# Performance work log

Hardware: AMD Instinct MI355X
Metric: run time of the kernel (lower is better)

Reference implementation:

```python
import jax, jax.numpy as jnp
import numpy as np

N = 8192
NUM_FEAT = 512
NUM_HIDDENS = 128


def _mlp_params(key, fin, fh):
    k1, k2, k3, k4 = jax.random.split(key, 4)
    s1 = 1.0 / np.sqrt(fin)
    s2 = 1.0 / np.sqrt(fh)
    W1 = jax.random.uniform(k1, (fin, fh), jnp.float32, -s1, s1)
    b1 = jax.random.uniform(k2, (fh,), jnp.float32, -s1, s1)
    W2 = jax.random.uniform(k3, (fh, fh), jnp.float32, -s2, s2)
    b2 = jax.random.uniform(k4, (fh,), jnp.float32, -s2, s2)
    return W1, b1, W2, b2


def setup_inputs() -> dict:
    key = jax.random.key(0)
    ks = jax.random.split(key, 9)
    feat = jax.random.normal(ks[0], (N, NUM_FEAT), jnp.float32)
    adj = jax.random.uniform(ks[1], (N, N), jnp.float32)
    aa = jax.random.uniform(ks[2], (N, N), jnp.float32)
    mod = jax.random.normal(ks[3], (N, N), jnp.float32)
    Wl1, bl1, Wl2, bl2 = _mlp_params(ks[4], NUM_FEAT, NUM_HIDDENS)
    Wu1, bu1, Wu2, bu2 = _mlp_params(ks[5], NUM_FEAT, NUM_HIDDENS)
    Wa1, ba1, Wa2, ba2 = _mlp_params(ks[6], NUM_FEAT, NUM_HIDDENS)
    Wm1, bm1, Wm2, bm2 = _mlp_params(ks[7], NUM_FEAT, NUM_HIDDENS)
    ws = jnp.zeros((3,), jnp.float32)  # nn.init.zeros_(weighted_sum)
    return dict(feat=feat, adj=adj, aa=aa, mod=mod,
                Wl1=Wl1, bl1=bl1, Wl2=Wl2, bl2=bl2,
                Wu1=Wu1, bu1=bu1, Wu2=Wu2, bu2=bu2,
                Wa1=Wa1, ba1=ba1, Wa2=Wa2, ba2=ba2,
                Wm1=Wm1, bm1=bm1, Wm2=Wm2, bm2=bm2,
                ws=ws)


def _latent(feat, W1, b1, W2, b2):
    h = jax.nn.relu(feat @ W1 + b1)
    return h @ W2 + b2  # [N, H]


def reference(feat, adj, aa, mod,
              Wl1, bl1, Wl2, bl2,
              Wu1, bu1, Wu2, bu2,
              Wa1, ba1, Wa2, ba2,
              Wm1, bm1, Wm2, bm2, ws):
    lat_link = _latent(feat, Wl1, bl1, Wl2, bl2)
    lat_aa = _latent(feat, Wa1, ba1, Wa2, ba2)
    lat_mod = _latent(feat, Wm1, bm1, Wm2, bm2)
    lat_unlink = _latent(feat, Wu1, bu1, Wu2, bu2)

    link_ctx = jax.nn.sigmoid(lat_link @ lat_link.T)          # [N, N]
    aa_ctx = jax.nn.sigmoid((lat_aa @ lat_aa.T) * aa)         # [N, N]
    mod_ctx = jax.nn.sigmoid((lat_mod @ lat_mod.T) * mod)     # [N, N]

    w = jax.nn.softmax(ws)  # [3]
    # cat(..., dim=2) @ w  ==  weighted sum of the three contexts
    weight_link = w[0] * link_ctx + w[1] * aa_ctx + w[2] * mod_ctx

    weight_unlink = jax.nn.sigmoid(lat_unlink @ lat_unlink.T)
    return (weight_link - weight_unlink) * adj + weight_unlink
```

## Files before the change

kernel.cpp:

```cpp
#include <hip/hip_runtime.h>


typedef __attribute__((ext_vector_type(8))) short short8;
typedef __attribute__((ext_vector_type(4))) float f32x4;

__device__ __forceinline__ unsigned short f2bf(float x) {
  union { float f; unsigned u; } v; v.f = x;
  unsigned u = v.u + 0x7FFFu + ((v.u >> 16) & 1u);
  return (unsigned short)(u >> 16);
}

__device__ __forceinline__ float sigf(float x) {
  float e = __builtin_amdgcn_exp2f(-1.4426950408889634f * x);
  return __builtin_amdgcn_rcpf(1.0f + e);
}

__device__ __forceinline__ void gload_lds16(const float* g, float* l) {
  __builtin_amdgcn_global_load_lds(
      (const __attribute__((address_space(1))) void*)g,
      (__attribute__((address_space(3))) void*)l, 16, 0, 0);
}
__device__ __forceinline__ void gload_lds16u(const unsigned short* g, unsigned short* l) {
  __builtin_amdgcn_global_load_lds(
      (const __attribute__((address_space(1))) void*)g,
      (__attribute__((address_space(3))) void*)l, 16, 0, 0);
}

__device__ __forceinline__ unsigned lds_off(const void* p) {
  return (unsigned)(uintptr_t)(const __attribute__((address_space(3))) void*)p;
}
__device__ __forceinline__ f32x4 ds_read_f32x4(unsigned a) {
  f32x4 d;
  asm volatile("ds_read_b128 %0, %1" : "=v"(d) : "v"(a));
  return d;
}
__device__ __forceinline__ short8 ds_read_frag(unsigned a) {
  short8 d;
  asm volatile("ds_read_b128 %0, %1" : "=v"(d) : "v"(a));
  return d;
}

__global__ __launch_bounds__(256) void k_featfrag(const float* __restrict__ feat,
                                                  unsigned short* __restrict__ dst) {
  int t = blockIdx.x * 256 + threadIdx.x;
  int row = t >> 6, kc = t & 63;
  const float4* s = reinterpret_cast<const float4*>(feat + row * 512 + kc * 8);
  float4 v0 = s[0], v1 = s[1];
  short8 o;
  o[0] = f2bf(v0.x); o[1] = f2bf(v0.y); o[2] = f2bf(v0.z); o[3] = f2bf(v0.w);
  o[4] = f2bf(v1.x); o[5] = f2bf(v1.y); o[6] = f2bf(v1.z); o[7] = f2bf(v1.w);
  int mb = row >> 4, kk = kc >> 2;
  int lane = ((kc & 3) << 4) | (row & 15);
  *reinterpret_cast<short8*>(dst + ((size_t)((mb * 16 + kk) * 64 + lane)) * 8) = o;
}

__global__ __launch_bounds__(256) void k_wfrag(
    const float* __restrict__ w1_0, const float* __restrict__ w1_1,
    const float* __restrict__ w1_2, const float* __restrict__ w1_3,
    const float* __restrict__ w2_0, const float* __restrict__ w2_1,
    const float* __restrict__ w2_2, const float* __restrict__ w2_3,
    unsigned short* __restrict__ w1f, unsigned short* __restrict__ w2f) {
  int t = blockIdx.x * 256 + threadIdx.x;
  if (t < 32768) {
    int lane = t & 63, nb = (t >> 6) & 7, kk = (t >> 9) & 15, g = t >> 13;
    const float* W = g == 0 ? w1_0 : g == 1 ? w1_1 : g == 2 ? w1_2 : w1_3;
    int q = lane >> 4, r = lane & 15;
    int col = nb * 16 + r;
    short8 o;
#pragma unroll
    for (int j = 0; j < 8; ++j) o[j] = f2bf(W[(kk * 32 + q * 8 + j) * 128 + col]);
    *reinterpret_cast<short8*>(w1f + (size_t)t * 8) = o;
  } else if (t < 40960) {
    int t2 = t - 32768;
    int lane = t2 & 63, nb = (t2 >> 6) & 7, kk = (t2 >> 9) & 3, g = t2 >> 11;
    const float* W = g == 0 ? w2_0 : g == 1 ? w2_1 : g == 2 ? w2_2 : w2_3;
    int q = lane >> 4, r = lane & 15;
    int col = nb * 16 + r;
    short8 o;
#pragma unroll
    for (int j = 0; j < 8; ++j) o[j] = f2bf(W[(kk * 32 + q * 8 + j) * 128 + col]);
    *reinterpret_cast<short8*>(w2f + (size_t)t2 * 8) = o;
  }
}

__global__ __launch_bounds__(256) void k_gemm1(
    const unsigned short* __restrict__ featf, const unsigned short* __restrict__ w1f,
    const float* __restrict__ b1_0, const float* __restrict__ b1_1,
    const float* __restrict__ b1_2, const float* __restrict__ b1_3,
    unsigned short* __restrict__ hfrag) {
  int bi = blockIdx.x, g = blockIdx.y;
  int lane = threadIdx.x & 63, w = threadIdx.x >> 6;
  int wm = w >> 1, wn = w & 1;
  int q = lane >> 4, r = lane & 15;
  int mbase = 8 * bi + 4 * wm;

  f32x4 s[4][4];
#pragma unroll
  for (int mi = 0; mi < 4; ++mi)
#pragma unroll
    for (int nj = 0; nj < 4; ++nj) s[mi][nj] = (f32x4){0.f, 0.f, 0.f, 0.f};

  for (int kk = 0; kk < 16; ++kk) {
    short8 a[4], b[4];
#pragma unroll
    for (int mi = 0; mi < 4; ++mi)
      a[mi] = *reinterpret_cast<const short8*>(
          featf + ((size_t)(((mbase + mi) * 16 + kk) * 64 + lane)) * 8);
#pragma unroll
    for (int nj = 0; nj < 4; ++nj)
      b[nj] = *reinterpret_cast<const short8*>(
          w1f + ((size_t)(((g * 16 + kk) * 8 + 4 * wn + nj) * 64 + lane)) * 8);
#pragma unroll
    for (int mi = 0; mi < 4; ++mi)
#pragma unroll
      for (int nj = 0; nj < 4; ++nj)
        s[mi][nj] = __builtin_amdgcn_mfma_f32_16x16x32_bf16(a[mi], b[nj], s[mi][nj], 0, 0, 0);
  }

  const float* b1 = g == 0 ? b1_0 : g == 1 ? b1_1 : g == 2 ? b1_2 : b1_3;
#pragma unroll
  for (int nj = 0; nj < 4; ++nj) {
    int cl = 64 * wn + 16 * nj + r;
    float bias = b1[cl];
    int Cg = 128 * g + cl;
    int kkd = Cg >> 5;
    int lane2hi = ((Cg >> 3) & 3) << 4;
    int j2 = Cg & 7;
#pragma unroll
    for (int mi = 0; mi < 4; ++mi) {
#pragma unroll
      for (int v = 0; v < 4; ++v) {
        int R = 128 * bi + 64 * wm + 16 * mi + 4 * q + v;
        float val = fmaxf(s[mi][nj][v] + bias, 0.0f);
        int mb = R >> 4;
        int lane2 = lane2hi | (R & 15);
        hfrag[((size_t)((mb * 16 + kkd) * 64 + lane2)) * 8 + j2] = f2bf(val);
      }
    }
  }
}

__global__ __launch_bounds__(256) void k_gemm2(
    const unsigned short* __restrict__ hfrag, const unsigned short* __restrict__ w2f,
    const float* __restrict__ b2_0, const float* __restrict__ b2_1,
    const float* __restrict__ b2_2, const float* __restrict__ b2_3,
    unsigned short* __restrict__ latf) {
  int bi = blockIdx.x, g = blockIdx.y;
  int lane = threadIdx.x & 63, w = threadIdx.x >> 6;
  int wm = w >> 1, wn = w & 1;
  int q = lane >> 4, r = lane & 15;
  int mbase = 8 * bi + 4 * wm;

  f32x4 s[4][4];
#pragma unroll
  for (int mi = 0; mi < 4; ++mi)
#pragma unroll
    for (int nj = 0; nj < 4; ++nj) s[mi][nj] = (f32x4){0.f, 0.f, 0.f, 0.f};

#pragma unroll
  for (int kk = 0; kk < 4; ++kk) {
    short8 a[4], b[4];
#pragma unroll
    for (int mi = 0; mi < 4; ++mi)
      a[mi] = *reinterpret_cast<const short8*>(
          hfrag + ((size_t)(((mbase + mi) * 16 + 4 * g + kk) * 64 + lane)) * 8);
#pragma unroll
    for (int nj = 0; nj < 4; ++nj)
      b[nj] = *reinterpret_cast<const short8*>(
          w2f + ((size_t)(((g * 4 + kk) * 8 + 4 * wn + nj) * 64 + lane)) * 8);
#pragma unroll
    for (int mi = 0; mi < 4; ++mi)
#pragma unroll
      for (int nj = 0; nj < 4; ++nj)
        s[mi][nj] = __builtin_amdgcn_mfma_f32_16x16x32_bf16(a[mi], b[nj], s[mi][nj], 0, 0, 0);
  }

  const float* b2 = g == 0 ? b2_0 : g == 1 ? b2_1 : g == 2 ? b2_2 : b2_3;
#pragma unroll
  for (int nj = 0; nj < 4; ++nj) {
    int cl = 64 * wn + 16 * nj + r;
    float bias = b2[cl];
    int kkd = cl >> 5;
    int lane2hi = ((cl >> 3) & 3) << 4;
    int j2 = cl & 7;
#pragma unroll
    for (int mi = 0; mi < 4; ++mi) {
#pragma unroll
      for (int v = 0; v < 4; ++v) {
        int R = 128 * bi + 64 * wm + 16 * mi + 4 * q + v;
        float val = s[mi][nj][v] + bias;
        int mb = R >> 4;
        int lane2 = lane2hi | (R & 15);
        latf[((size_t)(((g * 512 + mb) * 4 + kkd) * 64 + lane2)) * 8 + j2] = f2bf(val);
      }
    }
  }
}


#define FJLD(dst, p, OFF) \
  asm volatile("global_load_dwordx4 %0, %1, off offset:" OFF : "=v"(dst) : "v"(p))

#define LOADFJ(F, TJ)                                                         \
  do {                                                                        \
    const unsigned short* _b = latf + (size_t)(TJ) * 2048 + (size_t)lane * 8; \
    FJLD(F[0][0], _b, "0");    FJLD(F[0][1], _b, "1024");                     \
    FJLD(F[0][2], _b, "2048"); FJLD(F[0][3], _b, "3072");                     \
    _b += GS;                                                                 \
    FJLD(F[1][0], _b, "0");    FJLD(F[1][1], _b, "1024");                     \
    FJLD(F[1][2], _b, "2048"); FJLD(F[1][3], _b, "3072");                     \
    _b += GS;                                                                 \
    FJLD(F[2][0], _b, "0");    FJLD(F[2][1], _b, "1024");                     \
    FJLD(F[2][2], _b, "2048"); FJLD(F[2][3], _b, "3072");                     \
    _b += GS;                                                                 \
    FJLD(F[3][0], _b, "0");    FJLD(F[3][1], _b, "1024");                     \
    FJLD(F[3][2], _b, "2048"); FJLD(F[3][3], _b, "3072");                     \
  } while (0)

#define GRAM(FC, G, OUTV)                                                     \
  do {                                                                        \
    short8 _f0 = ds_read_frag(fib + (G * 4 + 0) * 1024u + l16);               \
    short8 _f1 = ds_read_frag(fib + (G * 4 + 1) * 1024u + l16);               \
    short8 _f2 = ds_read_frag(fib + (G * 4 + 2) * 1024u + l16);               \
    short8 _f3 = ds_read_frag(fib + (G * 4 + 3) * 1024u + l16);               \
    asm volatile("s_waitcnt lgkmcnt(0)" ::: "memory");                        \
    __builtin_amdgcn_sched_barrier(0);                                        \
    f32x4 _sg = (f32x4){0.f, 0.f, 0.f, 0.f};                                  \
    _sg = __builtin_amdgcn_mfma_f32_16x16x32_bf16(FC[G][0], _f0, _sg, 0, 0, 0); \
    _sg = __builtin_amdgcn_mfma_f32_16x16x32_bf16(FC[G][1], _f1, _sg, 0, 0, 0); \
    _sg = __builtin_amdgcn_mfma_f32_16x16x32_bf16(FC[G][2], _f2, _sg, 0, 0, 0); \
    _sg = __builtin_amdgcn_mfma_f32_16x16x32_bf16(FC[G][3], _f3, _sg, 0, 0, 0); \
    OUTV = _sg;                                                               \
  } while (0)

#define STEP(S, FC, FN)                                                       \
  do {                                                                        \
    int _sn = ((S) + 1 < 32) ? (S) + 1 : 31;                                  \
    LOADFJ(FN, cs * 128 + _sn * 4 + w);                                       \
    __builtin_amdgcn_sched_barrier(0);                                        \
    {                                                                         \
      int _sf = ((S) + 2 < 32) ? (S) + 2 : 31;                                \
      fill_ew(_sf, ((S) + 2) % 3);                                            \
    }                                                                         \
    __builtin_amdgcn_sched_barrier(0);                                        \
    asm volatile("s_waitcnt vmcnt(23)" ::: "memory");                         \
    __builtin_amdgcn_sched_barrier(0);                                        \
    unsigned _ea = ewb + (unsigned)(((S) % 3) * 3072 + rdidx) * 4u;           \
    f32x4 ewa = ds_read_f32x4(_ea);                                           \
    f32x4 ewm = ds_read_f32x4(_ea + 4096u);                                   \
    f32x4 ewj = ds_read_f32x4(_ea + 8192u);                                   \
    f32x4 sg, o4;                                                             \
    GRAM(FC, 0, sg);                                                          \
    o4[0] = w0 * sigf(sg[0]); o4[1] = w0 * sigf(sg[1]);                       \
    o4[2] = w0 * sigf(sg[2]); o4[3] = w0 * sigf(sg[3]);                       \
    GRAM(FC, 1, sg);                                                          \
    o4[0] += w1 * sigf(sg[0] * ewa[0]); o4[1] += w1 * sigf(sg[1] * ewa[1]);   \
    o4[2] += w1 * sigf(sg[2] * ewa[2]); o4[3] += w1 * sigf(sg[3] * ewa[3]);   \
    GRAM(FC, 2, sg);                                                          \
    o4[0] += w2 * sigf(sg[0] * ewm[0]); o4[1] += w2 * sigf(sg[1] * ewm[1]);   \
    o4[2] += w2 * sigf(sg[2] * ewm[2]); o4[3] += w2 * sigf(sg[3] * ewm[3]);   \
    GRAM(FC, 3, sg);                                                          \
    f32x4 res;                                                                \
    { float u0 = sigf(sg[0]), u1 = sigf(sg[1]), u2 = sigf(sg[2]), u3 = sigf(sg[3]); \
      res[0] = ewj[0] * (o4[0] - u0) + u0; res[1] = ewj[1] * (o4[1] - u1) + u1; \
      res[2] = ewj[2] * (o4[2] - u2) + u2; res[3] = ewj[3] * (o4[3] - u3) + u3; } \
    {                                                                         \
      float* _op = out + (size_t)(bi * 16 + r) * 8192 + (size_t)cs * 2048     \
                   + (S) * 64 + 16 * w + 4 * q;                               \
      asm volatile("global_store_dwordx4 %0, %1, off" ::"v"(_op), "v"(res)    \
                   : "memory");                                               \
    }                                                                         \
    asm volatile("s_waitcnt vmcnt(21)" ::: "memory");                         \
    __builtin_amdgcn_s_barrier();                                             \
  } while (0)

__global__ __launch_bounds__(256, 2) void k_ctx(
    const unsigned short* __restrict__ latf,
    const float* __restrict__ adj, const float* __restrict__ aa,
    const float* __restrict__ mod, const float* __restrict__ wsv,
    float* __restrict__ out) {
  __shared__ unsigned short fi_lds[8192];
  __shared__ float ew_lds[3][3][1024];

  const int bid = blockIdx.x;
  const int cs = bid & 3;
  const int bi = bid >> 2;
  const int lane = threadIdx.x & 63, w = threadIdx.x >> 6;
  const int q = lane >> 4, r = lane & 15;

  float s0w = wsv[0], s1w = wsv[1], s2w = wsv[2];
  float mx = fmaxf(fmaxf(s0w, s1w), s2w);
  float e0 = __builtin_amdgcn_exp2f(1.4426950408889634f * (s0w - mx));
  float e1 = __builtin_amdgcn_exp2f(1.4426950408889634f * (s1w - mx));
  float e2 = __builtin_amdgcn_exp2f(1.4426950408889634f * (s2w - mx));
  float inv = __builtin_amdgcn_rcpf(e0 + e1 + e2);
  float w0 = e0 * inv, w1 = e1 * inv, w2 = e2 * inv;

  const size_t GS = (size_t)512 * 2048;

  auto fill_ew = [&](int s2, int buf) {
    int rl = lane >> 4;
    int fx = lane & 15;
    int lrow = 4 * w + rl;
    int scol = 4 * (fx ^ (lrow & 7));
    size_t ga = (size_t)(bi * 16 + lrow) * 8192 + (size_t)cs * 2048
              + (size_t)s2 * 64 + scol;
    gload_lds16(aa + ga, &ew_lds[buf][0][w * 256]);
    gload_lds16(mod + ga, &ew_lds[buf][1][w * 256]);
    gload_lds16(adj + ga, &ew_lds[buf][2][w * 256]);
  };

#pragma unroll
  for (int kk = 0; kk < 4; ++kk)
    gload_lds16u(latf + GS * w + (size_t)(bi * 4 + kk) * 512 + lane * 8,
                 &fi_lds[(w * 4 + kk) * 512]);
  fill_ew(0, 0);
  fill_ew(1, 1);

  short8 fjA[4][4], fjB[4][4];
  LOADFJ(fjA, cs * 128 + 0 * 4 + w);
  asm volatile("s_waitcnt vmcnt(0)" ::: "memory");
  __builtin_amdgcn_s_barrier();

  const unsigned fib = lds_off(fi_lds);
  const unsigned ewb = lds_off(&ew_lds[0][0][0]);
  const unsigned l16 = (unsigned)lane * 16u;
  const unsigned rdidx = (unsigned)(r * 64 + ((16 * w + 4 * q) ^ (4 * (r & 7))));

  for (int s = 0; s < 32; s += 2) {
    STEP(s, fjA, fjB);
    STEP(s + 1, fjB, fjA);
  }
}

extern "C" void kernel_launch(void* const* d_in, const int* in_sizes, int n_in,
                              void* d_out, int out_size, void* d_ws, size_t ws_size,
                              hipStream_t stream) {
  const float* feat = (const float*)d_in[0];
  const float* adj  = (const float*)d_in[1];
  const float* aa   = (const float*)d_in[2];
  const float* mod  = (const float*)d_in[3];
  const float* W1g[4] = {(const float*)d_in[4], (const float*)d_in[12],
                         (const float*)d_in[16], (const float*)d_in[8]};
  const float* b1g[4] = {(const float*)d_in[5], (const float*)d_in[13],
                         (const float*)d_in[17], (const float*)d_in[9]};
  const float* W2g[4] = {(const float*)d_in[6], (const float*)d_in[14],
                         (const float*)d_in[18], (const float*)d_in[10]};
  const float* b2g[4] = {(const float*)d_in[7], (const float*)d_in[15],
                         (const float*)d_in[19], (const float*)d_in[11]};
  const float* wsv = (const float*)d_in[20];
  float* out = (float*)d_out;

  unsigned short* featf = (unsigned short*)d_ws;
  unsigned short* hfrag = featf + 4194304;
  unsigned short* latf  = hfrag + 4194304;
  unsigned short* w1f   = latf + 4194304;
  unsigned short* w2f   = w1f + 262144;
  if (ws_size < 25821184) return;

  k_featfrag<<<2048, 256, 0, stream>>>(feat, featf);
  k_wfrag<<<160, 256, 0, stream>>>(W1g[0], W1g[1], W1g[2], W1g[3],
                                   W2g[0], W2g[1], W2g[2], W2g[3], w1f, w2f);
  k_gemm1<<<dim3(64, 4), 256, 0, stream>>>(featf, w1f, b1g[0], b1g[1], b1g[2], b1g[3], hfrag);
  k_gemm2<<<dim3(64, 4), 256, 0, stream>>>(hfrag, w2f, b2g[0], b2g[1], b2g[2], b2g[3], latf);
  k_ctx<<<2048, 256, 0, stream>>>(latf, adj, aa, mod, wsv, out);
}
```

Measured before the change: 366.2 us.

## Load elementwise tiles directly to registers and stream latent fragments per group

Drops the LDS staging buffer for the aa/mod/adj tiles. Each lane now loads its own 16-byte slices straight into registers, double-buffered across steps, and the per-step block barrier is gone. The latent j-fragments are no longer double-buffered whole (32 short8 registers). They are streamed one gram group at a time, with fine-grained vmcnt waits interleaved with the MFMAs. This cuts register pressure so launch bounds can rise from 2 to 4 blocks per CU. The cost is less prefetch lead time for the latent loads, and a risk of exposed global latency if occupancy does not hide it.

```diff
diff --git a/kernel.cpp b/kernel.cpp
--- a/kernel.cpp
+++ b/kernel.cpp
@@ -15,11 +15,6 @@
   return __builtin_amdgcn_rcpf(1.0f + e);
 }
 
-__device__ __forceinline__ void gload_lds16(const float* g, float* l) {
-  __builtin_amdgcn_global_load_lds(
-      (const __attribute__((address_space(1))) void*)g,
-      (__attribute__((address_space(3))) void*)l, 16, 0, 0);
-}
 __device__ __forceinline__ void gload_lds16u(const unsigned short* g, unsigned short* l) {
   __builtin_amdgcn_global_load_lds(
       (const __attribute__((address_space(1))) void*)g,
@@ -28,11 +23,6 @@
 
 __device__ __forceinline__ unsigned lds_off(const void* p) {
   return (unsigned)(uintptr_t)(const __attribute__((address_space(3))) void*)p;
-}
-__device__ __forceinline__ f32x4 ds_read_f32x4(unsigned a) {
-  f32x4 d;
-  asm volatile("ds_read_b128 %0, %1" : "=v"(d) : "v"(a));
-  return d;
 }
 __device__ __forceinline__ short8 ds_read_frag(unsigned a) {
   short8 d;
@@ -198,93 +188,92 @@
 }
 
 
-#define FJLD(dst, p, OFF) \
+#define VLD4(dst, p, OFF) \
   asm volatile("global_load_dwordx4 %0, %1, off offset:" OFF : "=v"(dst) : "v"(p))
 
-#define LOADFJ(F, TJ)                                                         \
+#define LOADG(F, G)                                                           \
   do {                                                                        \
-    const unsigned short* _b = latf + (size_t)(TJ) * 2048 + (size_t)lane * 8; \
-    FJLD(F[0][0], _b, "0");    FJLD(F[0][1], _b, "1024");                     \
-    FJLD(F[0][2], _b, "2048"); FJLD(F[0][3], _b, "3072");                     \
-    _b += GS;                                                                 \
-    FJLD(F[1][0], _b, "0");    FJLD(F[1][1], _b, "1024");                     \
-    FJLD(F[1][2], _b, "2048"); FJLD(F[1][3], _b, "3072");                     \
-    _b += GS;                                                                 \
-    FJLD(F[2][0], _b, "0");    FJLD(F[2][1], _b, "1024");                     \
-    FJLD(F[2][2], _b, "2048"); FJLD(F[2][3], _b, "3072");                     \
-    _b += GS;                                                                 \
-    FJLD(F[3][0], _b, "0");    FJLD(F[3][1], _b, "1024");                     \
-    FJLD(F[3][2], _b, "2048"); FJLD(F[3][3], _b, "3072");                     \
+    const unsigned short* _p = fjbase + (size_t)(G) * GS;                     \
+    VLD4(F[0], _p, "0");    VLD4(F[1], _p, "1024");                           \
+    VLD4(F[2], _p, "2048"); VLD4(F[3], _p, "3072");                           \
   } while (0)
 
-#define GRAM(FC, G, OUTV)                                                     \
+#define GRAMG(SG, F, G)                                                       \
   do {                                                                        \
-    short8 _f0 = ds_read_frag(fib + (G * 4 + 0) * 1024u + l16);               \
-    short8 _f1 = ds_read_frag(fib + (G * 4 + 1) * 1024u + l16);               \
-    short8 _f2 = ds_read_frag(fib + (G * 4 + 2) * 1024u + l16);               \
-    short8 _f3 = ds_read_frag(fib + (G * 4 + 3) * 1024u + l16);               \
+    short8 _i0 = ds_read_frag(fib + ((G) * 4 + 0) * 1024u + l16);             \
+    short8 _i1 = ds_read_frag(fib + ((G) * 4 + 1) * 1024u + l16);             \
+    short8 _i2 = ds_read_frag(fib + ((G) * 4 + 2) * 1024u + l16);             \
+    short8 _i3 = ds_read_frag(fib + ((G) * 4 + 3) * 1024u + l16);             \
     asm volatile("s_waitcnt lgkmcnt(0)" ::: "memory");                        \
     __builtin_amdgcn_sched_barrier(0);                                        \
-    f32x4 _sg = (f32x4){0.f, 0.f, 0.f, 0.f};                                  \
-    _sg = __builtin_amdgcn_mfma_f32_16x16x32_bf16(FC[G][0], _f0, _sg, 0, 0, 0); \
-    _sg = __builtin_amdgcn_mfma_f32_16x16x32_bf16(FC[G][1], _f1, _sg, 0, 0, 0); \
-    _sg = __builtin_amdgcn_mfma_f32_16x16x32_bf16(FC[G][2], _f2, _sg, 0, 0, 0); \
-    _sg = __builtin_amdgcn_mfma_f32_16x16x32_bf16(FC[G][3], _f3, _sg, 0, 0, 0); \
-    OUTV = _sg;                                                               \
+    SG = (f32x4){0.f, 0.f, 0.f, 0.f};                                         \
+    SG = __builtin_amdgcn_mfma_f32_16x16x32_bf16(F[0], _i0, SG, 0, 0, 0);     \
+    SG = __builtin_amdgcn_mfma_f32_16x16x32_bf16(F[1], _i1, SG, 0, 0, 0);     \
+    SG = __builtin_amdgcn_mfma_f32_16x16x32_bf16(F[2], _i2, SG, 0, 0, 0);     \
+    SG = __builtin_amdgcn_mfma_f32_16x16x32_bf16(F[3], _i3, SG, 0, 0, 0);     \
   } while (0)
 
-#define STEP(S, FC, FN)                                                       \
+#define STEP(S, EWCa, EWCm, EWCj, EWNa, EWNm, EWNj)                           \
   do {                                                                        \
-    int _sn = ((S) + 1 < 32) ? (S) + 1 : 31;                                  \
-    LOADFJ(FN, cs * 128 + _sn * 4 + w);                                       \
-    __builtin_amdgcn_sched_barrier(0);                                        \
-    {                                                                         \
-      int _sf = ((S) + 2 < 32) ? (S) + 2 : 31;                                \
-      fill_ew(_sf, ((S) + 2) % 3);                                            \
-    }                                                                         \
-    __builtin_amdgcn_sched_barrier(0);                                        \
-    asm volatile("s_waitcnt vmcnt(23)" ::: "memory");                         \
-    __builtin_amdgcn_sched_barrier(0);                                        \
-    unsigned _ea = ewb + (unsigned)(((S) % 3) * 3072 + rdidx) * 4u;           \
-    f32x4 ewa = ds_read_f32x4(_ea);                                           \
-    f32x4 ewm = ds_read_f32x4(_ea + 4096u);                                   \
-    f32x4 ewj = ds_read_f32x4(_ea + 8192u);                                   \
+    const unsigned short* fjbase =                                            \
+        latf + (size_t)(cb0 + (S) * 4 + w) * 2048 + (size_t)lane * 8;         \
+    short8 fjA[4], fjB[4];                                                    \
+    LOADG(fjA, 0);                                                            \
+    LOADG(fjB, 1);                                                            \
+    asm volatile("s_waitcnt vmcnt(4)" ::: "memory");   \
+    __builtin_amdgcn_sched_barrier(0);                                        \
     f32x4 sg, o4;                                                             \
-    GRAM(FC, 0, sg);                                                          \
+    GRAMG(sg, fjA, 0);                                                        \
+    LOADG(fjA, 2);                                      \
     o4[0] = w0 * sigf(sg[0]); o4[1] = w0 * sigf(sg[1]);                       \
     o4[2] = w0 * sigf(sg[2]); o4[3] = w0 * sigf(sg[3]);                       \
-    GRAM(FC, 1, sg);                                                          \
-    o4[0] += w1 * sigf(sg[0] * ewa[0]); o4[1] += w1 * sigf(sg[1] * ewa[1]);   \
-    o4[2] += w1 * sigf(sg[2] * ewa[2]); o4[3] += w1 * sigf(sg[3] * ewa[3]);   \
-    GRAM(FC, 2, sg);                                                          \
-    o4[0] += w2 * sigf(sg[0] * ewm[0]); o4[1] += w2 * sigf(sg[1] * ewm[1]);   \
-    o4[2] += w2 * sigf(sg[2] * ewm[2]); o4[3] += w2 * sigf(sg[3] * ewm[3]);   \
-    GRAM(FC, 3, sg);                                                          \
+    asm volatile("s_waitcnt vmcnt(4)" ::: "memory");            \
+    __builtin_amdgcn_sched_barrier(0);                                        \
+    GRAMG(sg, fjB, 1);                                                        \
+    LOADG(fjB, 3);                                      \
+    o4[0] += w1 * sigf(sg[0] * EWCa[0]); o4[1] += w1 * sigf(sg[1] * EWCa[1]); \
+    o4[2] += w1 * sigf(sg[2] * EWCa[2]); o4[3] += w1 * sigf(sg[3] * EWCa[3]); \
+    asm volatile("s_waitcnt vmcnt(4)" ::: "memory");        \
+    __builtin_amdgcn_sched_barrier(0);                                        \
+    GRAMG(sg, fjA, 2);                                                        \
+    {                                 \
+      int _sn = ((S) + 1 < 32) ? (S) + 1 : (S);                               \
+      const float* _ea = aa + ewoff + (size_t)_sn * 64;                       \
+      const float* _em = mod + ewoff + (size_t)_sn * 64;                      \
+      const float* _ej = adj + ewoff + (size_t)_sn * 64;                      \
+      VLD4(EWNa, _ea, "0"); VLD4(EWNm, _em, "0"); VLD4(EWNj, _ej, "0");       \
+    }                                                                         \
+    o4[0] += w2 * sigf(sg[0] * EWCm[0]); o4[1] += w2 * sigf(sg[1] * EWCm[1]); \
+    o4[2] += w2 * sigf(sg[2] * EWCm[2]); o4[3] += w2 * sigf(sg[3] * EWCm[3]); \
+    asm volatile("s_waitcnt vmcnt(3)" ::: "memory");        \
+    __builtin_amdgcn_sched_barrier(0);                                        \
+    GRAMG(sg, fjB, 3);                                                        \
     f32x4 res;                                                                \
-    { float u0 = sigf(sg[0]), u1 = sigf(sg[1]), u2 = sigf(sg[2]), u3 = sigf(sg[3]); \
-      res[0] = ewj[0] * (o4[0] - u0) + u0; res[1] = ewj[1] * (o4[1] - u1) + u1; \
-      res[2] = ewj[2] * (o4[2] - u2) + u2; res[3] = ewj[3] * (o4[3] - u3) + u3; } \
     {                                                                         \
-      float* _op = out + (size_t)(bi * 16 + r) * 8192 + (size_t)cs * 2048     \
-                   + (S) * 64 + 16 * w + 4 * q;                               \
+      float u0 = sigf(sg[0]), u1 = sigf(sg[1]);                               \
+      float u2 = sigf(sg[2]), u3 = sigf(sg[3]);                               \
+      res[0] = EWCj[0] * (o4[0] - u0) + u0;                                   \
+      res[1] = EWCj[1] * (o4[1] - u1) + u1;                                   \
+      res[2] = EWCj[2] * (o4[2] - u2) + u2;                                   \
+      res[3] = EWCj[3] * (o4[3] - u3) + u3;                                   \
+    }                                                                         \
+    {                                                                         \
+      float* _op = out + ewoff + (size_t)(S) * 64;                            \
       asm volatile("global_store_dwordx4 %0, %1, off" ::"v"(_op), "v"(res)    \
                    : "memory");                                               \
     }                                                                         \
-    asm volatile("s_waitcnt vmcnt(21)" ::: "memory");                         \
-    __builtin_amdgcn_s_barrier();                                             \
   } while (0)
 
-__global__ __launch_bounds__(256, 2) void k_ctx(
+__global__ __launch_bounds__(256, 4) void k_ctx(
     const unsigned short* __restrict__ latf,
     const float* __restrict__ adj, const float* __restrict__ aa,
     const float* __restrict__ mod, const float* __restrict__ wsv,
     float* __restrict__ out) {
   __shared__ unsigned short fi_lds[8192];
-  __shared__ float ew_lds[3][3][1024];
 
   const int bid = blockIdx.x;
   const int cs = bid & 3;
-  const int bi = bid >> 2;
+  const int mb = bid >> 2;
   const int lane = threadIdx.x & 63, w = threadIdx.x >> 6;
   const int q = lane >> 4, r = lane & 15;
 
@@ -297,39 +286,30 @@
   float w0 = e0 * inv, w1 = e1 * inv, w2 = e2 * inv;
 
   const size_t GS = (size_t)512 * 2048;
-
-  auto fill_ew = [&](int s2, int buf) {
-    int rl = lane >> 4;
-    int fx = lane & 15;
-    int lrow = 4 * w + rl;
-    int scol = 4 * (fx ^ (lrow & 7));
-    size_t ga = (size_t)(bi * 16 + lrow) * 8192 + (size_t)cs * 2048
-              + (size_t)s2 * 64 + scol;
-    gload_lds16(aa + ga, &ew_lds[buf][0][w * 256]);
-    gload_lds16(mod + ga, &ew_lds[buf][1][w * 256]);
-    gload_lds16(adj + ga, &ew_lds[buf][2][w * 256]);
-  };
+  const int cb0 = cs * 128;
+
+  const size_t ewoff = (size_t)(mb * 16 + r) * 8192 + (size_t)cs * 2048
+                     + (size_t)(16 * w + 4 * q);
 
 #pragma unroll
   for (int kk = 0; kk < 4; ++kk)
-    gload_lds16u(latf + GS * w + (size_t)(bi * 4 + kk) * 512 + lane * 8,
+    gload_lds16u(latf + GS * w + (size_t)(mb * 4 + kk) * 512 + lane * 8,
                  &fi_lds[(w * 4 + kk) * 512]);
-  fill_ew(0, 0);
-  fill_ew(1, 1);
-
-  short8 fjA[4][4], fjB[4][4];
-  LOADFJ(fjA, cs * 128 + 0 * 4 + w);
+
+  f32x4 ewAa, ewAm, ewAj, ewBa, ewBm, ewBj;
+  VLD4(ewAa, (aa + ewoff), "0");
+  VLD4(ewAm, (mod + ewoff), "0");
+  VLD4(ewAj, (adj + ewoff), "0");
   asm volatile("s_waitcnt vmcnt(0)" ::: "memory");
   __builtin_amdgcn_s_barrier();
 
   const unsigned fib = lds_off(fi_lds);
-  const unsigned ewb = lds_off(&ew_lds[0][0][0]);
   const unsigned l16 = (unsigned)lane * 16u;
-  const unsigned rdidx = (unsigned)(r * 64 + ((16 * w + 4 * q) ^ (4 * (r & 7))));
-
+
+#pragma unroll 1
   for (int s = 0; s < 32; s += 2) {
-    STEP(s, fjA, fjB);
-    STEP(s + 1, fjB, fjA);
+    STEP(s, ewAa, ewAm, ewAj, ewBa, ewBm, ewBj);
+    STEP(s + 1, ewBa, ewBm, ewBj, ewAa, ewAm, ewAj);
   }
 }
 
```

After: 451.1 us. 1.23x slower.
